# Optimization experiments

Measured on AMD Instinct MI355X. Metric: run time of the kernel, lower is better.

Reference implementation:

```python
import jax, jax.numpy as jnp
import numpy as np

S, B, H = 2048, 16, 512      # seq_len, batch, hidden_size
L = 4096                     # total labels across batch
SMAX = 16                    # max span length
LAB = 256                    # label_size
V = 32000                    # len(voc)


def setup_inputs() -> dict:
    key = jax.random.key(0)
    ks = jax.random.split(key, 10)
    hidden = jax.random.normal(ks[0], (S, B, H), jnp.float32)
    begins = jax.random.randint(ks[1], (L,), 1, S - SMAX - 1)          # >=1 so begin-1 valid
    lens = jax.random.randint(ks[2], (L,), 1, SMAX + 1)                # span length in [1, SMAX]
    ends = begins + lens                                               # < S so hidden[end] valid
    bids = jax.random.randint(ks[3], (L,), 0, B)
    tags = jax.random.randint(ks[4], (L,), 0, V)
    sc = 0.02
    W1 = jax.random.normal(ks[5], (3 * H, LAB), jnp.float32) * sc
    b1 = jnp.zeros((LAB,), jnp.float32)
    W2 = jax.random.normal(ks[6], (LAB, LAB), jnp.float32) * sc
    b2 = jnp.zeros((LAB,), jnp.float32)
    Wo = jax.random.normal(ks[7], (LAB, V), jnp.float32) * sc
    bo = jnp.zeros((V,), jnp.float32)
    return dict(hidden=hidden, begins=begins, ends=ends, bids=bids, tags=tags,
                W1=W1, b1=b1, W2=W2, b2=b2, Wo=Wo, bo=bo)


def reference(hidden, begins, ends, bids, tags, W1, b1, W2, b2, Wo, bo):
    # --- batched span embed: gather + masked mean + boundary concat ---
    pos = begins[:, None] + jnp.arange(SMAX)            # [L, SMAX]
    valid = (pos < ends[:, None]).astype(hidden.dtype)  # [L, SMAX]
    posc = jnp.minimum(pos, S - 1)
    g = hidden[posc, bids[:, None]]                     # [L, SMAX, H] gather
    span_len = (ends - begins).astype(hidden.dtype)[:, None]
    mean = (g * valid[..., None]).sum(axis=1) / span_len           # [L, H]
    left = hidden[begins - 1, bids]                                 # [L, H]
    right = hidden[ends, bids]                                      # [L, H]
    span_emb = jnp.concatenate([left, mean, right], axis=-1)        # [L, 3H]
    # --- hidden2feature: Linear -> sigmoid -> Linear (dropout = eval identity) ---
    feat = jax.nn.sigmoid(span_emb @ W1 + b1) @ W2 + b2             # [L, LAB]
    # --- SoftmaxLoss: -log_softmax(h2o(feat)).gather(tags).mean() per label ---
    logp = jax.nn.log_softmax(feat @ Wo + bo, axis=-1)              # [L, V]
    per_label = -logp[jnp.arange(L), tags]                          # one tag per label
    return per_label.sum() / (L + 1e-5)
```

## Files before the change

kernel.cpp:

```cpp
#include <hip/hip_runtime.h>
#include <math.h>

#define S 2048
#define B 16
#define H 512
#define L 4096
#define SMAX 16
#define LAB 256
#define V 32000
#define NCH 250
#define LOG2E 1.44269504f

typedef __attribute__((ext_vector_type(8))) short short8;
typedef __attribute__((ext_vector_type(4))) float float4v;

__device__ inline ushort f2bf(float x) {
  union { float f; unsigned u; } c; c.f = x;
  unsigned r = c.u + 0x7fffu + ((c.u >> 16) & 1u);
  return (ushort)(r >> 16);
}
__device__ inline float bf2f(ushort h) {
  union { unsigned u; float f; } c; c.u = ((unsigned)h) << 16;
  return c.f;
}

__global__ __launch_bounds__(256) void spanb_kernel(
    const float* __restrict__ hidden, const int* __restrict__ begins,
    const int* __restrict__ ends, const int* __restrict__ bids,
    ushort* __restrict__ spanb) {
  int sub = threadIdx.x >> 7, t = threadIdx.x & 127;
  int l = blockIdx.x * 2 + sub;
  int b = bids[l], s0 = begins[l], s1 = ends[l];
  const float4* hidv = (const float4*)hidden;
  float4 lf = hidv[((size_t)(s0 - 1) * B + b) * 128 + t];
  float4 rf = hidv[((size_t)s1 * B + b) * 128 + t];
  float4 m = make_float4(0.f, 0.f, 0.f, 0.f);
  int len = s1 - s0;
  for (int j = 0; j < len; ++j) {
    float4 g = hidv[((size_t)(s0 + j) * B + b) * 128 + t];
    m.x += g.x; m.y += g.y; m.z += g.z; m.w += g.w;
  }
  float inv = 1.0f / (float)len;
  ushort* sp = spanb + (size_t)l * 1536;
  ushort4 u;
  u.x = f2bf(lf.x); u.y = f2bf(lf.y); u.z = f2bf(lf.z); u.w = f2bf(lf.w);
  *(ushort4*)&sp[t * 4] = u;
  u.x = f2bf(m.x * inv); u.y = f2bf(m.y * inv);
  u.z = f2bf(m.z * inv); u.w = f2bf(m.w * inv);
  *(ushort4*)&sp[512 + t * 4] = u;
  u.x = f2bf(rf.x); u.y = f2bf(rf.y); u.z = f2bf(rf.z); u.w = f2bf(rf.w);
  *(ushort4*)&sp[1024 + t * 4] = u;
}

__global__ __launch_bounds__(256) void tcast_kernel(
    const float* __restrict__ src, ushort* __restrict__ dst, int K, int N) {
  __shared__ ushort tile[64 * 72];
  int t = threadIdx.x;
  int n0 = blockIdx.x * 64;
  int k0 = blockIdx.y * 64;
  #pragma unroll
  for (int p = 0; p < 16; ++p) {
    int k = p * 4 + (t >> 6);
    int n = t & 63;
    tile[n * 72 + k] = f2bf(src[(size_t)(k0 + k) * N + n0 + n]);
  }
  __syncthreads();
  #pragma unroll
  for (int p = 0; p < 2; ++p) {
    int idx = p * 256 + t;
    int n = idx >> 3, c = idx & 7;
    *(uint4*)&dst[(size_t)(n0 + n) * K + k0 + c * 8] =
        *(const uint4*)&tile[n * 72 + c * 8];
  }
}

#define FST 72
__global__ __launch_bounds__(256, 2) void feat_mfma_kernel(
    const ushort* __restrict__ spanb, const ushort* __restrict__ W1b,
    const float* __restrict__ b1, const ushort* __restrict__ W2b,
    const float* __restrict__ b2, ushort* __restrict__ featb) {
  __shared__ ushort As[32 * FST];
  __shared__ ushort Bs[256 * FST];
  __shared__ ushort Hs[32 * 264];
  int tid = threadIdx.x;
  int w = tid >> 6, lane = tid & 63;
  int lr = lane & 15, lq = lane >> 4;
  int l0 = blockIdx.x * 32;

  float4v acc[2][4];
  float4v zero = {0.f, 0.f, 0.f, 0.f};
  #pragma unroll
  for (int mt = 0; mt < 2; ++mt)
    #pragma unroll
    for (int nt = 0; nt < 4; ++nt) acc[mt][nt] = zero;

  for (int s = 0; s < 24; ++s) {
    int ks = s * 64;
    __syncthreads();
    {
      int r = tid >> 3, c = tid & 7;
      *(uint4*)&As[r * FST + c * 8] =
          *(const uint4*)&spanb[(size_t)(l0 + r) * 1536 + ks + c * 8];
    }
    #pragma unroll
    for (int p = 0; p < 8; ++p) {
      int idx = p * 256 + tid;
      int r = idx >> 3, c = idx & 7;
      *(uint4*)&Bs[r * FST + c * 8] =
          *(const uint4*)&W1b[(size_t)r * 1536 + ks + c * 8];
    }
    __syncthreads();
    #pragma unroll
    for (int kk = 0; kk < 2; ++kk) {
      short8 af[2], bf[4];
      #pragma unroll
      for (int mt = 0; mt < 2; ++mt)
        af[mt] = *(const short8*)&As[(mt * 16 + lr) * FST + kk * 32 + lq * 8];
      #pragma unroll
      for (int nt = 0; nt < 4; ++nt)
        bf[nt] = *(const short8*)
            &Bs[(w * 64 + nt * 16 + lr) * FST + kk * 32 + lq * 8];
      #pragma unroll
      for (int mt = 0; mt < 2; ++mt)
        #pragma unroll
        for (int nt = 0; nt < 4; ++nt)
          acc[mt][nt] = __builtin_amdgcn_mfma_f32_16x16x32_bf16(
              af[mt], bf[nt], acc[mt][nt], 0, 0, 0);
    }
  }

  {
    float b1v[4];
    #pragma unroll
    for (int nt = 0; nt < 4; ++nt) b1v[nt] = b1[w * 64 + nt * 16 + lr];
    #pragma unroll
    for (int mt = 0; mt < 2; ++mt)
      #pragma unroll
      for (int nt = 0; nt < 4; ++nt)
        #pragma unroll
        for (int r = 0; r < 4; ++r) {
          int row = mt * 16 + lq * 4 + r;
          int col = w * 64 + nt * 16 + lr;
          float h = 1.0f / (1.0f + __expf(-(acc[mt][nt][r] + b1v[nt])));
          Hs[row * 264 + col] = f2bf(h);
        }
  }

  float4v acc2[2][4];
  #pragma unroll
  for (int mt = 0; mt < 2; ++mt)
    #pragma unroll
    for (int nt = 0; nt < 4; ++nt) acc2[mt][nt] = zero;

  for (int s = 0; s < 4; ++s) {
    int ks = s * 64;
    __syncthreads();
    #pragma unroll
    for (int p = 0; p < 8; ++p) {
      int idx = p * 256 + tid;
      int r = idx >> 3, c = idx & 7;
      *(uint4*)&Bs[r * FST + c * 8] =
          *(const uint4*)&W2b[(size_t)r * 256 + ks + c * 8];
    }
    __syncthreads();
    #pragma unroll
    for (int kk = 0; kk < 2; ++kk) {
      short8 af[2], bf[4];
      #pragma unroll
      for (int mt = 0; mt < 2; ++mt)
        af[mt] = *(const short8*)
            &Hs[(mt * 16 + lr) * 264 + ks + kk * 32 + lq * 8];
      #pragma unroll
      for (int nt = 0; nt < 4; ++nt)
        bf[nt] = *(const short8*)
            &Bs[(w * 64 + nt * 16 + lr) * FST + kk * 32 + lq * 8];
      #pragma unroll
      for (int mt = 0; mt < 2; ++mt)
        #pragma unroll
        for (int nt = 0; nt < 4; ++nt)
          acc2[mt][nt] = __builtin_amdgcn_mfma_f32_16x16x32_bf16(
              af[mt], bf[nt], acc2[mt][nt], 0, 0, 0);
    }
  }

  {
    float b2v[4];
    #pragma unroll
    for (int nt = 0; nt < 4; ++nt) b2v[nt] = b2[w * 64 + nt * 16 + lr];
    #pragma unroll
    for (int mt = 0; mt < 2; ++mt)
      #pragma unroll
      for (int nt = 0; nt < 4; ++nt)
        #pragma unroll
        for (int r = 0; r < 4; ++r) {
          int row = mt * 16 + lq * 4 + r;
          int col = w * 64 + nt * 16 + lr;
          featb[(size_t)(l0 + row) * 256 + col] =
              f2bf(acc2[mt][nt][r] + b2v[nt]);
        }
  }
}

#define BST2 264
__global__ __launch_bounds__(256, 2) void logits3_kernel(
    const ushort* __restrict__ featb, const ushort* __restrict__ Wob,
    const float* __restrict__ bo, float* __restrict__ pz) {
  __shared__ ushort Blds[128 * BST2];
  int tid = threadIdx.x;
  int ch = blockIdx.x;
  int l0 = blockIdx.y * 256;
  int v0 = ch * 128;
  int w = tid >> 6, lane = tid & 63;
  int lr = lane & 15, lq = lane >> 4;

  {
    const uint4* src = (const uint4*)(Wob + (size_t)v0 * 256);
    #pragma unroll
    for (int p = 0; p < 16; ++p) {
      int idx = p * 256 + tid;
      int r = idx >> 5, c = idx & 31;
      *(uint4*)&Blds[r * BST2 + c * 8] = src[idx];
    }
  }
  __syncthreads();

  float4v acc[4][8];
  float4v zero = {0.f, 0.f, 0.f, 0.f};
  #pragma unroll
  for (int mt = 0; mt < 4; ++mt)
    #pragma unroll
    for (int nt = 0; nt < 8; ++nt) acc[mt][nt] = zero;

  const ushort* abase = featb + (size_t)(l0 + w * 64 + lr) * 256 + lq * 8;

  #pragma unroll
  for (int k = 0; k < 8; ++k) {
    short8 af[4];
    #pragma unroll
    for (int mt = 0; mt < 4; ++mt)
      af[mt] = *(const short8*)(abase + mt * 16 * 256 + k * 32);
    short8 bf[8];
    #pragma unroll
    for (int nt = 0; nt < 8; ++nt)
      bf[nt] = *(const short8*)&Blds[(nt * 16 + lr) * BST2 + k * 32 + lq * 8];
    #pragma unroll
    for (int mt = 0; mt < 4; ++mt)
      #pragma unroll
      for (int nt = 0; nt < 8; ++nt)
        acc[mt][nt] = __builtin_amdgcn_mfma_f32_16x16x32_bf16(
            af[mt], bf[nt], acc[mt][nt], 0, 0, 0);
  }

  float bov[8];
  #pragma unroll
  for (int nt = 0; nt < 8; ++nt)
    bov[nt] = bo[v0 + nt * 16 + lr] * LOG2E;
  float z[4][4];
  #pragma unroll
  for (int mt = 0; mt < 4; ++mt)
    #pragma unroll
    for (int r = 0; r < 4; ++r) z[mt][r] = 0.f;
  #pragma unroll
  for (int mt = 0; mt < 4; ++mt)
    #pragma unroll
    for (int nt = 0; nt < 8; ++nt)
      #pragma unroll
      for (int r = 0; r < 4; ++r)
        z[mt][r] += exp2f(fmaf(acc[mt][nt][r], LOG2E, bov[nt]));
  #pragma unroll
  for (int mt = 0; mt < 4; ++mt)
    #pragma unroll
    for (int r = 0; r < 4; ++r) {
      #pragma unroll
      for (int off = 1; off < 16; off <<= 1)
        z[mt][r] += __shfl_xor(z[mt][r], off);
    }
  if (lr == 0) {
    #pragma unroll
    for (int mt = 0; mt < 4; ++mt)
      #pragma unroll
      for (int r = 0; r < 4; ++r)
        pz[(size_t)ch * L + l0 + w * 64 + mt * 16 + lq * 4 + r] = z[mt][r];
  }
}

__global__ __launch_bounds__(256) void tag_kernel(
    const ushort* __restrict__ featb, const ushort* __restrict__ Wob,
    const float* __restrict__ bo, const int* __restrict__ tags,
    float* __restrict__ tagl) {
  int l = blockIdx.x * 4 + (threadIdx.x >> 6);
  int lane = threadIdx.x & 63;
  int tg = tags[l];
  ushort4 fa = *(const ushort4*)&featb[(size_t)l * 256 + lane * 4];
  ushort4 wa = *(const ushort4*)&Wob[(size_t)tg * 256 + lane * 4];
  float s = bf2f(fa.x) * bf2f(wa.x) + bf2f(fa.y) * bf2f(wa.y) +
            bf2f(fa.z) * bf2f(wa.z) + bf2f(fa.w) * bf2f(wa.w);
  #pragma unroll
  for (int off = 1; off < 64; off <<= 1) s += __shfl_xor(s, off);
  if (lane == 0) tagl[l] = s + bo[tg];
}

__global__ __launch_bounds__(256) void reduce_kernel(
    const float* __restrict__ pz, const float* __restrict__ tagl,
    float* __restrict__ out) {
  int l = blockIdx.x * 256 + threadIdx.x;
  float z = 0.f;
  for (int c = 0; c < NCH; ++c) z += pz[(size_t)c * L + l];
  float per = logf(z) - tagl[l];
  float v = per * (1.0f / (4096.0f + 1e-5f));
  #pragma unroll
  for (int off = 1; off < 64; off <<= 1) v += __shfl_xor(v, off);
  __shared__ float wsum[4];
  if ((threadIdx.x & 63) == 0) wsum[threadIdx.x >> 6] = v;
  __syncthreads();
  if (threadIdx.x == 0)
    atomicAdd(out, wsum[0] + wsum[1] + wsum[2] + wsum[3]);
}

extern "C" void kernel_launch(void* const* d_in, const int* in_sizes, int n_in,
                              void* d_out, int out_size, void* d_ws,
                              size_t ws_size, hipStream_t stream) {
  const float* hidden = (const float*)d_in[0];
  const int* begins = (const int*)d_in[1];
  const int* ends = (const int*)d_in[2];
  const int* bids = (const int*)d_in[3];
  const int* tags = (const int*)d_in[4];
  const float* W1 = (const float*)d_in[5];
  const float* b1 = (const float*)d_in[6];
  const float* W2 = (const float*)d_in[7];
  const float* b2 = (const float*)d_in[8];
  const float* Wo = (const float*)d_in[9];
  const float* bo = (const float*)d_in[10];
  float* out = (float*)d_out;

  ushort* featb = (ushort*)d_ws;
  ushort* Wob = featb + (size_t)L * 256;
  ushort* spanb = Wob + (size_t)V * 256;
  ushort* W1b = spanb + (size_t)L * 1536;
  ushort* W2b = W1b + (size_t)256 * 1536;
  float* pz = (float*)(W2b + (size_t)256 * 256);
  float* tagl = pz + (size_t)NCH * L;

  hipMemsetAsync(d_out, 0, sizeof(float), stream);
  spanb_kernel<<<L / 2, 256, 0, stream>>>(hidden, begins, ends, bids, spanb);
  tcast_kernel<<<dim3(4, 24), 256, 0, stream>>>(W1, W1b, 1536, LAB);
  tcast_kernel<<<dim3(4, 4), 256, 0, stream>>>(W2, W2b, LAB, LAB);
  tcast_kernel<<<dim3(500, 4), 256, 0, stream>>>(Wo, Wob, LAB, V);
  feat_mfma_kernel<<<128, 256, 0, stream>>>(spanb, W1b, b1, W2b, b2, featb);
  logits3_kernel<<<dim3(NCH, 16), 256, 0, stream>>>(featb, Wob, bo, pz);
  tag_kernel<<<L / 4, 256, 0, stream>>>(featb, Wob, bo, tags, tagl);
  reduce_kernel<<<L / 256, 256, 0, stream>>>(pz, tagl, out);
}
```

Measured before the change: 319.2 us.

## Merge cast and reduce kernels, shrink feat tiles, retile logits warps

The three weight-cast launches become one kernel with a flattened block index, and the tag-dot kernel is fused with the partition-sum reduction, which cuts launch count. The feature MLP kernel now handles 16 rows per block instead of 32, putting 256 blocks on the GPU instead of 128. The logits kernel splits warps 2x2 (128 rows by 64 vocab columns each) instead of 4x1, and writes partial sums row-major so the reduction reads contiguously. The cost is that each feat block re-reads the full W1 for half as many rows, and the logits warps now hold 8x4 accumulators, which adds register pressure.

```diff
diff --git a/kernel.cpp b/kernel.cpp
--- a/kernel.cpp
+++ b/kernel.cpp
@@ -52,12 +52,24 @@
   *(ushort4*)&sp[1024 + t * 4] = u;
 }
 
-__global__ __launch_bounds__(256) void tcast_kernel(
-    const float* __restrict__ src, ushort* __restrict__ dst, int K, int N) {
+__global__ __launch_bounds__(256) void tcast3_kernel(
+    const float* __restrict__ Wo, ushort* __restrict__ Wob,
+    const float* __restrict__ W1, ushort* __restrict__ W1b,
+    const float* __restrict__ W2, ushort* __restrict__ W2b) {
   __shared__ ushort tile[64 * 72];
+  int id = blockIdx.x;
+  const float* src; ushort* dst; int K, N, n0, k0;
+  if (id < 2000) {
+    src = Wo; dst = Wob; K = 256; N = V;
+    n0 = (id % 500) * 64; k0 = (id / 500) * 64;
+  } else if (id < 2096) {
+    int i = id - 2000; src = W1; dst = W1b; K = 1536; N = 256;
+    n0 = (i & 3) * 64; k0 = (i >> 2) * 64;
+  } else {
+    int i = id - 2096; src = W2; dst = W2b; K = 256; N = 256;
+    n0 = (i & 3) * 64; k0 = (i >> 2) * 64;
+  }
   int t = threadIdx.x;
-  int n0 = blockIdx.x * 64;
-  int k0 = blockIdx.y * 64;
   #pragma unroll
   for (int p = 0; p < 16; ++p) {
     int k = p * 4 + (t >> 6);
@@ -79,25 +91,23 @@
     const ushort* __restrict__ spanb, const ushort* __restrict__ W1b,
     const float* __restrict__ b1, const ushort* __restrict__ W2b,
     const float* __restrict__ b2, ushort* __restrict__ featb) {
-  __shared__ ushort As[32 * FST];
+  __shared__ ushort As[16 * FST];
   __shared__ ushort Bs[256 * FST];
-  __shared__ ushort Hs[32 * 264];
+  __shared__ ushort Hs[16 * 264];
   int tid = threadIdx.x;
   int w = tid >> 6, lane = tid & 63;
   int lr = lane & 15, lq = lane >> 4;
-  int l0 = blockIdx.x * 32;
-
-  float4v acc[2][4];
+  int l0 = blockIdx.x * 16;
+
+  float4v acc[4];
   float4v zero = {0.f, 0.f, 0.f, 0.f};
   #pragma unroll
-  for (int mt = 0; mt < 2; ++mt)
-    #pragma unroll
-    for (int nt = 0; nt < 4; ++nt) acc[mt][nt] = zero;
+  for (int nt = 0; nt < 4; ++nt) acc[nt] = zero;
 
   for (int s = 0; s < 24; ++s) {
     int ks = s * 64;
     __syncthreads();
-    {
+    if (tid < 128) {
       int r = tid >> 3, c = tid & 7;
       *(uint4*)&As[r * FST + c * 8] =
           *(const uint4*)&spanb[(size_t)(l0 + r) * 1536 + ks + c * 8];
@@ -112,20 +122,16 @@
     __syncthreads();
     #pragma unroll
     for (int kk = 0; kk < 2; ++kk) {
-      short8 af[2], bf[4];
-      #pragma unroll
-      for (int mt = 0; mt < 2; ++mt)
-        af[mt] = *(const short8*)&As[(mt * 16 + lr) * FST + kk * 32 + lq * 8];
+      short8 af = *(const short8*)&As[lr * FST + kk * 32 + lq * 8];
+      short8 bf[4];
       #pragma unroll
       for (int nt = 0; nt < 4; ++nt)
         bf[nt] = *(const short8*)
             &Bs[(w * 64 + nt * 16 + lr) * FST + kk * 32 + lq * 8];
       #pragma unroll
-      for (int mt = 0; mt < 2; ++mt)
-        #pragma unroll
-        for (int nt = 0; nt < 4; ++nt)
-          acc[mt][nt] = __builtin_amdgcn_mfma_f32_16x16x32_bf16(
-              af[mt], bf[nt], acc[mt][nt], 0, 0, 0);
+      for (int nt = 0; nt < 4; ++nt)
+        acc[nt] = __builtin_amdgcn_mfma_f32_16x16x32_bf16(af, bf[nt],
+                                                          acc[nt], 0, 0, 0);
     }
   }
 
@@ -134,23 +140,17 @@
     #pragma unroll
     for (int nt = 0; nt < 4; ++nt) b1v[nt] = b1[w * 64 + nt * 16 + lr];
     #pragma unroll
-    for (int mt = 0; mt < 2; ++mt)
-      #pragma unroll
-      for (int nt = 0; nt < 4; ++nt)
-        #pragma unroll
-        for (int r = 0; r < 4; ++r) {
-          int row = mt * 16 + lq * 4 + r;
-          int col = w * 64 + nt * 16 + lr;
-          float h = 1.0f / (1.0f + __expf(-(acc[mt][nt][r] + b1v[nt])));
-          Hs[row * 264 + col] = f2bf(h);
-        }
-  }
-
-  float4v acc2[2][4];
-  #pragma unroll
-  for (int mt = 0; mt < 2; ++mt)
-    #pragma unroll
-    for (int nt = 0; nt < 4; ++nt) acc2[mt][nt] = zero;
+    for (int nt = 0; nt < 4; ++nt)
+      #pragma unroll
+      for (int r = 0; r < 4; ++r) {
+        float h = 1.0f / (1.0f + __expf(-(acc[nt][r] + b1v[nt])));
+        Hs[(lq * 4 + r) * 264 + w * 64 + nt * 16 + lr] = f2bf(h);
+      }
+  }
+
+  float4v acc2[4];
+  #pragma unroll
+  for (int nt = 0; nt < 4; ++nt) acc2[nt] = zero;
 
   for (int s = 0; s < 4; ++s) {
     int ks = s * 64;
@@ -165,21 +165,16 @@
     __syncthreads();
     #pragma unroll
     for (int kk = 0; kk < 2; ++kk) {
-      short8 af[2], bf[4];
-      #pragma unroll
-      for (int mt = 0; mt < 2; ++mt)
-        af[mt] = *(const short8*)
-            &Hs[(mt * 16 + lr) * 264 + ks + kk * 32 + lq * 8];
+      short8 af = *(const short8*)&Hs[lr * 264 + ks + kk * 32 + lq * 8];
+      short8 bf[4];
       #pragma unroll
       for (int nt = 0; nt < 4; ++nt)
         bf[nt] = *(const short8*)
             &Bs[(w * 64 + nt * 16 + lr) * FST + kk * 32 + lq * 8];
       #pragma unroll
-      for (int mt = 0; mt < 2; ++mt)
-        #pragma unroll
-        for (int nt = 0; nt < 4; ++nt)
-          acc2[mt][nt] = __builtin_amdgcn_mfma_f32_16x16x32_bf16(
-              af[mt], bf[nt], acc2[mt][nt], 0, 0, 0);
+      for (int nt = 0; nt < 4; ++nt)
+        acc2[nt] = __builtin_amdgcn_mfma_f32_16x16x32_bf16(af, bf[nt],
+                                                           acc2[nt], 0, 0, 0);
     }
   }
 
@@ -188,21 +183,16 @@
     #pragma unroll
     for (int nt = 0; nt < 4; ++nt) b2v[nt] = b2[w * 64 + nt * 16 + lr];
     #pragma unroll
-    for (int mt = 0; mt < 2; ++mt)
-      #pragma unroll
-      for (int nt = 0; nt < 4; ++nt)
-        #pragma unroll
-        for (int r = 0; r < 4; ++r) {
-          int row = mt * 16 + lq * 4 + r;
-          int col = w * 64 + nt * 16 + lr;
-          featb[(size_t)(l0 + row) * 256 + col] =
-              f2bf(acc2[mt][nt][r] + b2v[nt]);
-        }
+    for (int nt = 0; nt < 4; ++nt)
+      #pragma unroll
+      for (int r = 0; r < 4; ++r)
+        featb[(size_t)(l0 + lq * 4 + r) * 256 + w * 64 + nt * 16 + lr] =
+            f2bf(acc2[nt][r] + b2v[nt]);
   }
 }
 
 #define BST2 264
-__global__ __launch_bounds__(256, 2) void logits3_kernel(
+__global__ __launch_bounds__(256, 2) void logits5_kernel(
     const ushort* __restrict__ featb, const ushort* __restrict__ Wob,
     const float* __restrict__ bo, float* __restrict__ pz) {
   __shared__ ushort Blds[128 * BST2];
@@ -211,6 +201,7 @@
   int l0 = blockIdx.y * 256;
   int v0 = ch * 128;
   int w = tid >> 6, lane = tid & 63;
+  int wr = w >> 1, wc = w & 1;
   int lr = lane & 15, lq = lane >> 4;
 
   {
@@ -224,97 +215,94 @@
   }
   __syncthreads();
 
-  float4v acc[4][8];
+  float4v acc[8][4];
   float4v zero = {0.f, 0.f, 0.f, 0.f};
   #pragma unroll
-  for (int mt = 0; mt < 4; ++mt)
-    #pragma unroll
-    for (int nt = 0; nt < 8; ++nt) acc[mt][nt] = zero;
-
-  const ushort* abase = featb + (size_t)(l0 + w * 64 + lr) * 256 + lq * 8;
+  for (int mt = 0; mt < 8; ++mt)
+    #pragma unroll
+    for (int nt = 0; nt < 4; ++nt) acc[mt][nt] = zero;
+
+  const ushort* abase = featb + (size_t)(l0 + wr * 128 + lr) * 256 + lq * 8;
+  const ushort* bbase = Blds + (wc * 64 + lr) * BST2 + lq * 8;
 
   #pragma unroll
   for (int k = 0; k < 8; ++k) {
-    short8 af[4];
-    #pragma unroll
-    for (int mt = 0; mt < 4; ++mt)
+    short8 af[8];
+    #pragma unroll
+    for (int mt = 0; mt < 8; ++mt)
       af[mt] = *(const short8*)(abase + mt * 16 * 256 + k * 32);
-    short8 bf[8];
-    #pragma unroll
-    for (int nt = 0; nt < 8; ++nt)
-      bf[nt] = *(const short8*)&Blds[(nt * 16 + lr) * BST2 + k * 32 + lq * 8];
-    #pragma unroll
-    for (int mt = 0; mt < 4; ++mt)
-      #pragma unroll
-      for (int nt = 0; nt < 8; ++nt)
+    short8 bf[4];
+    #pragma unroll
+    for (int nt = 0; nt < 4; ++nt)
+      bf[nt] = *(const short8*)(bbase + nt * 16 * BST2 + k * 32);
+    #pragma unroll
+    for (int mt = 0; mt < 8; ++mt)
+      #pragma unroll
+      for (int nt = 0; nt < 4; ++nt)
         acc[mt][nt] = __builtin_amdgcn_mfma_f32_16x16x32_bf16(
             af[mt], bf[nt], acc[mt][nt], 0, 0, 0);
   }
 
-  float bov[8];
-  #pragma unroll
-  for (int nt = 0; nt < 8; ++nt)
-    bov[nt] = bo[v0 + nt * 16 + lr] * LOG2E;
-  float z[4][4];
-  #pragma unroll
-  for (int mt = 0; mt < 4; ++mt)
-    #pragma unroll
-    for (int r = 0; r < 4; ++r) z[mt][r] = 0.f;
-  #pragma unroll
-  for (int mt = 0; mt < 4; ++mt)
-    #pragma unroll
-    for (int nt = 0; nt < 8; ++nt)
+  float bov[4];
+  #pragma unroll
+  for (int nt = 0; nt < 4; ++nt)
+    bov[nt] = bo[v0 + wc * 64 + nt * 16 + lr] * LOG2E;
+  #pragma unroll
+  for (int mt = 0; mt < 8; ++mt) {
+    float z[4] = {0.f, 0.f, 0.f, 0.f};
+    #pragma unroll
+    for (int nt = 0; nt < 4; ++nt)
       #pragma unroll
       for (int r = 0; r < 4; ++r)
-        z[mt][r] += exp2f(fmaf(acc[mt][nt][r], LOG2E, bov[nt]));
-  #pragma unroll
-  for (int mt = 0; mt < 4; ++mt)
+        z[r] += exp2f(fmaf(acc[mt][nt][r], LOG2E, bov[nt]));
     #pragma unroll
     for (int r = 0; r < 4; ++r) {
       #pragma unroll
       for (int off = 1; off < 16; off <<= 1)
-        z[mt][r] += __shfl_xor(z[mt][r], off);
-    }
-  if (lr == 0) {
-    #pragma unroll
-    for (int mt = 0; mt < 4; ++mt)
+        z[r] += __shfl_xor(z[r], off);
+    }
+    if (lr == 0) {
       #pragma unroll
       for (int r = 0; r < 4; ++r)
-        pz[(size_t)ch * L + l0 + w * 64 + mt * 16 + lq * 4 + r] = z[mt][r];
-  }
-}
-
-__global__ __launch_bounds__(256) void tag_kernel(
-    const ushort* __restrict__ featb, const ushort* __restrict__ Wob,
-    const float* __restrict__ bo, const int* __restrict__ tags,
-    float* __restrict__ tagl) {
-  int l = blockIdx.x * 4 + (threadIdx.x >> 6);
-  int lane = threadIdx.x & 63;
-  int tg = tags[l];
-  ushort4 fa = *(const ushort4*)&featb[(size_t)l * 256 + lane * 4];
-  ushort4 wa = *(const ushort4*)&Wob[(size_t)tg * 256 + lane * 4];
-  float s = bf2f(fa.x) * bf2f(wa.x) + bf2f(fa.y) * bf2f(wa.y) +
-            bf2f(fa.z) * bf2f(wa.z) + bf2f(fa.w) * bf2f(wa.w);
-  #pragma unroll
-  for (int off = 1; off < 64; off <<= 1) s += __shfl_xor(s, off);
-  if (lane == 0) tagl[l] = s + bo[tg];
-}
-
-__global__ __launch_bounds__(256) void reduce_kernel(
-    const float* __restrict__ pz, const float* __restrict__ tagl,
-    float* __restrict__ out) {
-  int l = blockIdx.x * 256 + threadIdx.x;
-  float z = 0.f;
-  for (int c = 0; c < NCH; ++c) z += pz[(size_t)c * L + l];
-  float per = logf(z) - tagl[l];
-  float v = per * (1.0f / (4096.0f + 1e-5f));
-  #pragma unroll
-  for (int off = 1; off < 64; off <<= 1) v += __shfl_xor(v, off);
-  __shared__ float wsum[4];
-  if ((threadIdx.x & 63) == 0) wsum[threadIdx.x >> 6] = v;
+        pz[(size_t)(l0 + wr * 128 + mt * 16 + lq * 4 + r) * 512 +
+           ch * 2 + wc] = z[r];
+    }
+  }
+}
+
+__global__ __launch_bounds__(256) void tagreduce_kernel(
+    const float* __restrict__ pz, const ushort* __restrict__ featb,
+    const ushort* __restrict__ Wob, const float* __restrict__ bo,
+    const int* __restrict__ tags, float* __restrict__ out) {
+  int w = threadIdx.x >> 6, lane = threadIdx.x & 63;
+  float acc = 0.f;
+  for (int i = 0; i < 16; ++i) {
+    int l = blockIdx.x * 64 + w * 16 + i;
+    const float* row = pz + (size_t)l * 512;
+    float z = 0.f;
+    #pragma unroll
+    for (int j = 0; j < 8; ++j) {
+      int idx = j * 64 + lane;
+      z += (idx < 2 * NCH) ? row[idx] : 0.f;
+    }
+    int tg = tags[l];
+    ushort4 fa = *(const ushort4*)&featb[(size_t)l * 256 + lane * 4];
+    ushort4 wa = *(const ushort4*)&Wob[(size_t)tg * 256 + lane * 4];
+    float d = bf2f(fa.x) * bf2f(wa.x) + bf2f(fa.y) * bf2f(wa.y) +
+              bf2f(fa.z) * bf2f(wa.z) + bf2f(fa.w) * bf2f(wa.w);
+    #pragma unroll
+    for (int off = 1; off < 64; off <<= 1) {
+      z += __shfl_xor(z, off);
+      d += __shfl_xor(d, off);
+    }
+    if (lane == 0) acc += logf(z) - (d + bo[tg]);
+  }
+  __shared__ float ws4[4];
+  if (lane == 0) ws4[w] = acc;
   __syncthreads();
   if (threadIdx.x == 0)
-    atomicAdd(out, wsum[0] + wsum[1] + wsum[2] + wsum[3]);
+    atomicAdd(out,
+              (ws4[0] + ws4[1] + ws4[2] + ws4[3]) * (1.0f / (4096.0f + 1e-5f)));
 }
 
 extern "C" void kernel_launch(void* const* d_in, const int* in_sizes, int n_in,
@@ -339,15 +327,11 @@
   ushort* W1b = spanb + (size_t)L * 1536;
   ushort* W2b = W1b + (size_t)256 * 1536;
   float* pz = (float*)(W2b + (size_t)256 * 256);
-  float* tagl = pz + (size_t)NCH * L;
 
   hipMemsetAsync(d_out, 0, sizeof(float), stream);
   spanb_kernel<<<L / 2, 256, 0, stream>>>(hidden, begins, ends, bids, spanb);
-  tcast_kernel<<<dim3(4, 24), 256, 0, stream>>>(W1, W1b, 1536, LAB);
-  tcast_kernel<<<dim3(4, 4), 256, 0, stream>>>(W2, W2b, LAB, LAB);
-  tcast_kernel<<<dim3(500, 4), 256, 0, stream>>>(Wo, Wob, LAB, V);
-  feat_mfma_kernel<<<128, 256, 0, stream>>>(spanb, W1b, b1, W2b, b2, featb);
-  logits3_kernel<<<dim3(NCH, 16), 256, 0, stream>>>(featb, Wob, bo, pz);
-  tag_kernel<<<L / 4, 256, 0, stream>>>(featb, Wob, bo, tags, tagl);
-  reduce_kernel<<<L / 256, 256, 0, stream>>>(pz, tagl, out);
-}
+  tcast3_kernel<<<2112, 256, 0, stream>>>(Wo, Wob, W1, W1b, W2, W2b);
+  feat_mfma_kernel<<<L / 16, 256, 0, stream>>>(spanb, W1b, b1, W2b, b2, featb);
+  logits5_kernel<<<dim3(NCH, 16), 256, 0, stream>>>(featb, Wob, bo, pz);
+  tagreduce_kernel<<<64, 256, 0, stream>>>(pz, featb, Wob, bo, tags, out);
+}
```

After: 358.1 us. 12.2% more time.
